# Performance work log

Measured on AMD Instinct MI355X. Metric: run time of the kernel, lower is better.

Reference implementation:

```python
import jax, jax.numpy as jnp
import numpy as np

DIM = 1024
DEPTH = 4
HEADS = 16
DHEAD = 64
INNER = HEADS * DHEAD  # 1024
FF = 4 * DIM           # 4096
SCALE = DHEAD ** -0.5
LS_INIT = 0.1          # LayerScale init_eps for depth <= 18


def _layernorm(x, w, b):
    mu = jnp.mean(x, axis=-1, keepdims=True)
    var = jnp.mean((x - mu) ** 2, axis=-1, keepdims=True)
    return (x - mu) / jnp.sqrt(var + 1e-5) * w + b


def setup_inputs() -> dict:
    key = jax.random.key(0)
    ks = jax.random.split(key, 6)
    s = 0.02
    return {
        "x": jax.random.normal(ks[0], (2, 1024, DIM), dtype=jnp.float32),
        "ln1_w": jnp.ones((DEPTH, DIM), jnp.float32),
        "ln1_b": jnp.zeros((DEPTH, DIM), jnp.float32),
        "w_qkv": jax.random.normal(ks[1], (DEPTH, DIM, 3 * INNER), jnp.float32) * s,
        "w_out": jax.random.normal(ks[2], (DEPTH, INNER, DIM), jnp.float32) * s,
        "b_out": jnp.zeros((DEPTH, DIM), jnp.float32),
        "ls1": jnp.full((DEPTH, DIM), LS_INIT, jnp.float32),
        "ln2_w": jnp.ones((DEPTH, DIM), jnp.float32),
        "ln2_b": jnp.zeros((DEPTH, DIM), jnp.float32),
        "w_ff1": jax.random.normal(ks[3], (DEPTH, DIM, 2 * FF), jnp.float32) * s,
        "b_ff1": jnp.zeros((DEPTH, 2 * FF), jnp.float32),
        "w_ff2": jax.random.normal(ks[4], (DEPTH, FF, DIM), jnp.float32) * s,
        "b_ff2": jnp.zeros((DEPTH, DIM), jnp.float32),
        "ls2": jnp.full((DEPTH, DIM), LS_INIT, jnp.float32),
    }


def _block(x, p):
    (ln1w, ln1b, wqkv, wout, bout, ls1,
     ln2w, ln2b, wff1, bff1, wff2, bff2, ls2) = p
    b, n, _ = x.shape
    # --- PreNorm + Attention (non-causal, no mask) + LayerScale, residual ---
    h = _layernorm(x, ln1w, ln1b)
    qkv = h @ wqkv                                   # [b, n, 3*inner]
    q, k, v = jnp.split(qkv, 3, axis=-1)
    def heads(t):
        return t.reshape(b, n, HEADS, DHEAD).transpose(0, 2, 1, 3)  # b h n d
    q, k, v = heads(q) * SCALE, heads(k), heads(v)
    dots = jnp.einsum("bhid,bhjd->bhij", q, k)       # full O(n^2) scores
    attn = jax.nn.softmax(dots, axis=-1)
    o = jnp.einsum("bhij,bhjd->bhid", attn, v)
    o = o.transpose(0, 2, 1, 3).reshape(b, n, INNER)
    o = o @ wout + bout
    x = x + o * ls1
    # --- PreNorm + GEGLU FeedForward + LayerScale, residual ---
    h = _layernorm(x, ln2w, ln2b)
    u = h @ wff1 + bff1                              # [b, n, 2*FF]
    a, g = jnp.split(u, 2, axis=-1)
    ff = (a * jax.nn.gelu(g, approximate=False)) @ wff2 + bff2
    x = x + ff * ls2
    return x, None


def reference(x, ln1_w, ln1_b, w_qkv, w_out, b_out, ls1,
              ln2_w, ln2_b, w_ff1, b_ff1, w_ff2, b_ff2, ls2):
    ps = (ln1_w, ln1_b, w_qkv, w_out, b_out, ls1,
          ln2_w, ln2_b, w_ff1, b_ff1, w_ff2, b_ff2, ls2)
    out, _ = jax.lax.scan(_block, x, ps)
    return out
```

## Files before the change

### kernel.cpp

```cpp
#include <hip/hip_runtime.h>
#include <cstdint>
#include <cstddef>

typedef __bf16 bf16_t;
typedef __bf16 bf16x8 __attribute__((ext_vector_type(8)));
typedef __bf16 bf16x4 __attribute__((ext_vector_type(4)));
typedef float  f32x4  __attribute__((ext_vector_type(4)));

#define DEV __device__ __forceinline__

static constexpr int   BATCH = 2;
static constexpr int   NTOK  = 1024;
static constexpr int   DIM   = 1024;
static constexpr int   MROWS = BATCH * NTOK;
static constexpr float SCALE = 0.125f;

DEV void load_lds16(const bf16_t* g, bf16_t* s) {
  __builtin_amdgcn_global_load_lds(
      (const __attribute__((address_space(1))) void*)g,
      (__attribute__((address_space(3))) void*)s, 16, 0, 0);
}

DEV float wave_sum(float v) {
#pragma unroll
  for (int m = 1; m < 64; m <<= 1) v += __shfl_xor(v, m, 64);
  return v;
}
DEV float block_sum(float v, float* sb) {
  v = wave_sum(v);
  __syncthreads();
  if ((threadIdx.x & 63) == 0) sb[threadIdx.x >> 6] = v;
  __syncthreads();
  return sb[0] + sb[1] + sb[2] + sb[3];
}

template <int BM, int BN, int WR, int WC, int MODE>
__global__ __launch_bounds__(256) void gemm_bt(
    const bf16_t* __restrict__ A, long sA0, long sA1, int lda,
    const bf16_t* __restrict__ B, long sB0, long sB1, int ldb,
    void* __restrict__ Cv, long sC0, long sC1, int ldc,
    int K, float alpha, const float* __restrict__ bias,
    const float* __restrict__ ls, bf16_t* __restrict__ vtp) {
  constexpr int TM = BM / WR / 16;
  constexpr int TN = BN / WC / 16;
  __shared__ __attribute__((aligned(16))) bf16_t As[BM * 32];
  __shared__ __attribute__((aligned(16))) bf16_t Bs[BN * 32];

  const int tid  = threadIdx.x;
  const int lane = tid & 63, wave = tid >> 6;
  const int z  = blockIdx.z;
  const int zh = z >> 4, zl = z & 15;
  A += (size_t)zh * sA0 + (size_t)zl * sA1;
  B += (size_t)zh * sB0 + (size_t)zl * sB1;

  const int m0 = blockIdx.y * BM, n0 = blockIdx.x * BN;
  const int wm = (wave / WC) * (BM / WR);
  const int wn = (wave % WC) * (BN / WC);
  const int fm = lane & 15, quad = lane >> 4;

  f32x4 acc[TM][TN] = {};

  for (int k0 = 0; k0 < K; k0 += 32) {
#pragma unroll
    for (int c = tid; c < BM * 4; c += 256) {
      const int row = c >> 2, kc = (c & 3) << 3;
      load_lds16(A + (size_t)(m0 + row) * lda + k0 + kc, &As[c * 8]);
    }
#pragma unroll
    for (int c = tid; c < BN * 4; c += 256) {
      const int row = c >> 2, kc = (c & 3) << 3;
      load_lds16(B + (size_t)(n0 + row) * ldb + k0 + kc, &Bs[c * 8]);
    }
    __syncthreads();

    bf16x8 af[TM], bfr[TN];
#pragma unroll
    for (int i = 0; i < TM; ++i)
      af[i] = *(const bf16x8*)&As[(wm + i * 16 + fm) * 32 + quad * 8];
#pragma unroll
    for (int j = 0; j < TN; ++j)
      bfr[j] = *(const bf16x8*)&Bs[(wn + j * 16 + fm) * 32 + quad * 8];
#pragma unroll
    for (int i = 0; i < TM; ++i)
#pragma unroll
      for (int j = 0; j < TN; ++j)
        acc[i][j] = __builtin_amdgcn_mfma_f32_16x16x32_bf16(af[i], bfr[j],
                                                            acc[i][j], 0, 0, 0);
    __syncthreads();
  }

  const size_t coff = (size_t)zh * sC0 + (size_t)zl * sC1;
  if constexpr (MODE == 3) {
    bf16_t* C = (bf16_t*)Cv;
#pragma unroll
    for (int i = 0; i < TM; ++i) {
      const int rowb = m0 + wm + i * 16 + quad * 4;
#pragma unroll
      for (int p = 0; p < TN / 2; ++p) {
        const int   cf = ((n0 + wn) >> 1) + p * 16 + fm;
        const float ba = bias[cf], bg = bias[4096 + cf];
#pragma unroll
        for (int r = 0; r < 4; ++r) {
          const float a  = acc[i][2 * p][r] + ba;
          const float g  = acc[i][2 * p + 1][r] + bg;
          const float ge = 0.5f * g * (1.f + erff(g * 0.70710678118654752f));
          C[(size_t)(rowb + r) * ldc + cf] = (bf16_t)(a * ge);
        }
      }
    }
  } else if constexpr (MODE == 4) {
    bf16_t* C = (bf16_t*)Cv;
#pragma unroll
    for (int i = 0; i < TM; ++i) {
#pragma unroll
      for (int j = 0; j < TN; ++j) {
        const int col  = n0 + wn + j * 16 + fm;
        const int rowb = m0 + wm + i * 16 + quad * 4;
        if (col < 2048) {
#pragma unroll
          for (int r = 0; r < 4; ++r)
            C[(size_t)(rowb + r) * ldc + col] = (bf16_t)acc[i][j][r];
        } else {
          const int hh = (col - 2048) >> 6, d = (col - 2048) & 63;
#pragma unroll
          for (int r = 0; r < 4; ++r) {
            const int row = rowb + r, bb = row >> 10, tok = row & 1023;
            vtp[((size_t)(bb * 16 + hh) * 64 + d) * 1024 + tok] =
                (bf16_t)acc[i][j][r];
          }
        }
      }
    }
  } else {
#pragma unroll
    for (int i = 0; i < TM; ++i) {
#pragma unroll
      for (int j = 0; j < TN; ++j) {
        const int col  = n0 + wn + j * 16 + fm;
        const int rowb = m0 + wm + i * 16 + quad * 4;
#pragma unroll
        for (int r = 0; r < 4; ++r) {
          const float  v   = acc[i][j][r];
          const size_t idx = coff + (size_t)(rowb + r) * ldc + col;
          if constexpr (MODE == 0) {
            ((bf16_t*)Cv)[idx] = (bf16_t)(v * alpha);
          } else if constexpr (MODE == 1) {
            ((bf16_t*)Cv)[idx] = (bf16_t)(v + bias[col]);
          } else {
            float* C = (float*)Cv;
            C[idx]   = C[idx] + (v + bias[col]) * ls[col];
          }
        }
      }
    }
  }
}

__global__ __launch_bounds__(256) void flash_attn(
    const bf16_t* __restrict__ qkv,
    const bf16_t* __restrict__ vT,
    bf16_t* __restrict__ o) {
  constexpr int NT = 128;
  __shared__ __attribute__((aligned(16))) bf16_t Qs[2 * 64 * 32];
  __shared__ __attribute__((aligned(16))) bf16_t Ks[2 * NT * 32];
  __shared__ __attribute__((aligned(16))) bf16_t Vs[4 * 64 * 32];
  __shared__ __attribute__((aligned(16))) bf16_t Ps[4][4 * 16 * 32];

  const int tid = threadIdx.x, lane = tid & 63, wave = tid >> 6;
  const int fm = lane & 15, quad = lane >> 4;
  const int z = blockIdx.y, b = z >> 4, h = z & 15;
  const int q0 = blockIdx.x * 64;
  const bf16_t* qb  = qkv + (size_t)b * 1024 * 3072 + h * 64;
  const bf16_t* kb  = qb + 1024;
  const bf16_t* vtb = vT + (size_t)z * 64 * 1024;

  for (int c = tid; c < 512; c += 256) {
    const int kk = c >> 8, rr = (c >> 2) & 63, ii = c & 3;
    load_lds16(qb + (size_t)(q0 + rr) * 3072 + kk * 32 + ii * 8, &Qs[c * 8]);
  }
  __syncthreads();
  bf16x8 qf[2];
  qf[0] = *(const bf16x8*)&Qs[(wave * 16 + fm) * 32 + quad * 8];
  qf[1] = *(const bf16x8*)&Qs[64 * 32 + (wave * 16 + fm) * 32 + quad * 8];

  float mr[4], lr[4];
  f32x4 oacc[4];
#pragma unroll
  for (int r = 0; r < 4; ++r) { mr[r] = -1e30f; lr[r] = 0.f; }
#pragma unroll
  for (int t = 0; t < 4; ++t) oacc[t] = (f32x4){0.f, 0.f, 0.f, 0.f};

  for (int kv0 = 0; kv0 < 1024; kv0 += NT) {
    __syncthreads();
    for (int c = tid; c < NT * 8; c += 256) {
      const int kk = c >> 9, rr = (c >> 2) & 127, ii = c & 3;
      load_lds16(kb + (size_t)(kv0 + rr) * 3072 + kk * 32 + ii * 8, &Ks[c * 8]);
    }
    for (int c = tid; c < 1024; c += 256) {
      const int tc = c >> 8, rr = (c >> 2) & 63, ii = c & 3;
      load_lds16(vtb + (size_t)rr * 1024 + kv0 + tc * 32 + ii * 8, &Vs[c * 8]);
    }
    __syncthreads();

    f32x4 sc[8];
#pragma unroll
    for (int nt = 0; nt < 8; ++nt) {
      sc[nt] = (f32x4){0.f, 0.f, 0.f, 0.f};
#pragma unroll
      for (int kk = 0; kk < 2; ++kk) {
        const bf16x8 kf =
            *(const bf16x8*)&Ks[kk * NT * 32 + (nt * 16 + fm) * 32 + quad * 8];
        sc[nt] = __builtin_amdgcn_mfma_f32_16x16x32_bf16(qf[kk], kf, sc[nt],
                                                         0, 0, 0);
      }
    }
    float tmax[4] = {-1e30f, -1e30f, -1e30f, -1e30f};
#pragma unroll
    for (int nt = 0; nt < 8; ++nt)
#pragma unroll
      for (int r = 0; r < 4; ++r) {
        sc[nt][r] *= SCALE;
        tmax[r] = fmaxf(tmax[r], sc[nt][r]);
      }
#pragma unroll
    for (int m = 1; m < 16; m <<= 1)
#pragma unroll
      for (int r = 0; r < 4; ++r)
        tmax[r] = fmaxf(tmax[r], __shfl_xor(tmax[r], m, 64));
    float alpha[4], mn[4], ps[4];
#pragma unroll
    for (int r = 0; r < 4; ++r) {
      mn[r]    = fmaxf(mr[r], tmax[r]);
      alpha[r] = __expf(mr[r] - mn[r]);
      mr[r]    = mn[r];
      ps[r]    = 0.f;
    }
#pragma unroll
    for (int nt = 0; nt < 8; ++nt) {
      const int tcol = nt * 16 + fm, kk = tcol >> 5, tw = tcol & 31;
#pragma unroll
      for (int r = 0; r < 4; ++r) {
        const float p = __expf(sc[nt][r] - mn[r]);
        ps[r] += p;
        Ps[wave][kk * 512 + (quad * 4 + r) * 32 + tw] = (bf16_t)p;
      }
    }
#pragma unroll
    for (int m = 1; m < 16; m <<= 1)
#pragma unroll
      for (int r = 0; r < 4; ++r) ps[r] += __shfl_xor(ps[r], m, 64);
#pragma unroll
    for (int r = 0; r < 4; ++r) lr[r] = lr[r] * alpha[r] + ps[r];
#pragma unroll
    for (int t = 0; t < 4; ++t)
#pragma unroll
      for (int r = 0; r < 4; ++r) oacc[t][r] *= alpha[r];
    __builtin_amdgcn_s_waitcnt(0xC07F);
#pragma unroll
    for (int kk = 0; kk < 4; ++kk) {
      const bf16x8 af =
          *(const bf16x8*)&Ps[wave][kk * 512 + fm * 32 + quad * 8];
#pragma unroll
      for (int t = 0; t < 4; ++t) {
        const bf16x8 vf =
            *(const bf16x8*)&Vs[kk * 64 * 32 + (t * 16 + fm) * 32 + quad * 8];
        oacc[t] = __builtin_amdgcn_mfma_f32_16x16x32_bf16(af, vf, oacc[t],
                                                          0, 0, 0);
      }
    }
  }

  const size_t orow0 = (size_t)b * 1024 + q0 + wave * 16 + quad * 4;
#pragma unroll
  for (int t = 0; t < 4; ++t) {
    const int col = h * 64 + t * 16 + fm;
#pragma unroll
    for (int r = 0; r < 4; ++r)
      o[(orow0 + r) * 1024 + col] = (bf16_t)(oacc[t][r] / lr[r]);
  }
}

__global__ __launch_bounds__(256) void transpose_all(
    const float* __restrict__ wqkv, const float* __restrict__ wout,
    const float* __restrict__ wff1, const float* __restrict__ wff2,
    bf16_t* __restrict__ wqkvT, bf16_t* __restrict__ woutT,
    bf16_t* __restrict__ wff1T, bf16_t* __restrict__ wff2T, int l) {
  __shared__ float t[32][33];
  int bx = blockIdx.x;
  const float* W;
  bf16_t*      WT;
  int N, K;
  bool perm = false;
  if (bx < 3072) {
    W = wqkv + (size_t)l * 1024 * 3072; WT = wqkvT; K = 1024; N = 3072;
  } else if (bx < 4096) {
    bx -= 3072;
    W = wout + (size_t)l * 1024 * 1024; WT = woutT; K = 1024; N = 1024;
  } else if (bx < 12288) {
    bx -= 4096;
    W = wff1 + (size_t)l * 1024 * 8192; WT = wff1T; K = 1024; N = 8192;
    perm = true;
  } else {
    bx -= 12288;
    W = wff2 + (size_t)l * 4096 * 1024; WT = wff2T; K = 4096; N = 1024;
  }
  const int nbx = N >> 5;
  const int n0 = (bx % nbx) * 32, k0 = (bx / nbx) * 32;
  const int tx = threadIdx.x & 31, ty = threadIdx.x >> 5;
#pragma unroll
  for (int s = 0; s < 4; ++s)
    t[ty + 8 * s][tx] = W[(size_t)(k0 + ty + 8 * s) * N + n0 + tx];
  __syncthreads();
#pragma unroll
  for (int s = 0; s < 4; ++s) {
    const int n = n0 + ty + 8 * s;
    int r;
    if (perm)
      r = (n < 4096) ? (((n >> 4) << 5) + (n & 15))
                     : ((((n - 4096) >> 4) << 5) + 16 + (n & 15));
    else
      r = n;
    WT[(size_t)r * K + k0 + tx] = (bf16_t)t[tx][ty + 8 * s];
  }
}

__global__ __launch_bounds__(256) void ln_kernel(const float* __restrict__ x,
                                                 const float* __restrict__ w,
                                                 const float* __restrict__ b,
                                                 bf16_t* __restrict__ out) {
  __shared__ float sb[4];
  const int row = blockIdx.x, tid = threadIdx.x;
  const float4 v = ((const float4*)(x + (size_t)row * DIM))[tid];
  float s = v.x + v.y + v.z + v.w;
  s = block_sum(s, sb);
  const float mu = s * (1.f / DIM);
  const float dx = v.x - mu, dy = v.y - mu, dz = v.z - mu, dw = v.w - mu;
  float q = dx * dx + dy * dy + dz * dz + dw * dw;
  q = block_sum(q, sb);
  const float rstd = rsqrtf(q * (1.f / DIM) + 1e-5f);
  const float4 wv = ((const float4*)w)[tid];
  const float4 bv = ((const float4*)b)[tid];
  bf16x4 o;
  o[0] = (bf16_t)(dx * rstd * wv.x + bv.x);
  o[1] = (bf16_t)(dy * rstd * wv.y + bv.y);
  o[2] = (bf16_t)(dz * rstd * wv.z + bv.z);
  o[3] = (bf16_t)(dw * rstd * wv.w + bv.w);
  ((bf16x4*)(out + (size_t)row * DIM))[tid] = o;
}

extern "C" void kernel_launch(void* const* d_in, const int* in_sizes, int n_in,
                              void* d_out, int out_size, void* d_ws,
                              size_t ws_size, hipStream_t stream) {
  const float* x_in = (const float*)d_in[0];
  const float* ln1w = (const float*)d_in[1];
  const float* ln1b = (const float*)d_in[2];
  const float* wqkv = (const float*)d_in[3];
  const float* wout = (const float*)d_in[4];
  const float* bout = (const float*)d_in[5];
  const float* ls1  = (const float*)d_in[6];
  const float* ln2w = (const float*)d_in[7];
  const float* ln2b = (const float*)d_in[8];
  const float* wff1 = (const float*)d_in[9];
  const float* bff1 = (const float*)d_in[10];
  const float* wff2 = (const float*)d_in[11];
  const float* bff2 = (const float*)d_in[12];
  const float* ls2  = (const float*)d_in[13];
  float*       xout = (float*)d_out;

  char*   ws     = (char*)d_ws;
  bf16_t* wqkvT  = (bf16_t*)ws; ws += (size_t)3072 * 1024 * 2;
  bf16_t* woutT  = (bf16_t*)ws; ws += (size_t)1024 * 1024 * 2;
  bf16_t* wff1T  = (bf16_t*)ws; ws += (size_t)8192 * 1024 * 2;
  bf16_t* wff2T  = (bf16_t*)ws; ws += (size_t)1024 * 4096 * 2;
  bf16_t* h_bf   = (bf16_t*)ws; ws += (size_t)MROWS * 1024 * 2;
  bf16_t* qkv_bf = (bf16_t*)ws; ws += (size_t)MROWS * 3072 * 2;
  bf16_t* o_bf   = (bf16_t*)ws; ws += (size_t)MROWS * 1024 * 2;
  bf16_t* vT     = (bf16_t*)ws; ws += (size_t)32 * 64 * 1024 * 2;
  bf16_t* ff_bf  = (bf16_t*)ws; ws += (size_t)MROWS * 4096 * 2;
  if (ws_size < (size_t)(ws - (char*)d_ws)) return;

  hipMemcpyAsync(xout, x_in, (size_t)MROWS * DIM * 4,
                 hipMemcpyDeviceToDevice, stream);

  for (int l = 0; l < 4; ++l) {
    transpose_all<<<dim3(16384), 256, 0, stream>>>(
        wqkv, wout, wff1, wff2, wqkvT, woutT, wff1T, wff2T, l);

    ln_kernel<<<MROWS, 256, 0, stream>>>(xout, ln1w + l * 1024,
                                         ln1b + l * 1024, h_bf);
    gemm_bt<128, 128, 2, 2, 4><<<dim3(24, 16, 1), 256, 0, stream>>>(
        h_bf, 0, 0, 1024, wqkvT, 0, 0, 1024, qkv_bf, 0, 0, 3072, 1024, 1.f,
        nullptr, nullptr, vT);
    flash_attn<<<dim3(16, 32), 256, 0, stream>>>(qkv_bf, vT, o_bf);
    gemm_bt<64, 128, 1, 4, 2><<<dim3(8, 32, 1), 256, 0, stream>>>(
        o_bf, 0, 0, 1024, woutT, 0, 0, 1024, xout, 0, 0, 1024, 1024, 1.f,
        bout + l * 1024, ls1 + l * 1024, nullptr);

    ln_kernel<<<MROWS, 256, 0, stream>>>(xout, ln2w + l * 1024,
                                         ln2b + l * 1024, h_bf);
    gemm_bt<128, 128, 2, 2, 3><<<dim3(64, 16, 1), 256, 0, stream>>>(
        h_bf, 0, 0, 1024, wff1T, 0, 0, 1024, ff_bf, 0, 0, 4096, 1024, 1.f,
        bff1 + l * 8192, nullptr, nullptr);
    gemm_bt<64, 128, 1, 4, 2><<<dim3(8, 32, 1), 256, 0, stream>>>(
        ff_bf, 0, 0, 4096, wff2T, 0, 0, 4096, xout, 0, 0, 1024, 4096, 1.f,
        bff2 + l * 1024, ls2 + l * 1024, nullptr);
  }
}
```

Before: 1.179 ms.

## Add 256x256 ping-pong pipelined GEMM kernel for GEGLU FF1 projection

Measured after the change: 1.134 ms. 3.8% less time.

```diff
diff --git a/kernel.cpp b/kernel.cpp
--- a/kernel.cpp
+++ b/kernel.cpp
@@ -90,25 +90,7 @@
   }
 
   const size_t coff = (size_t)zh * sC0 + (size_t)zl * sC1;
-  if constexpr (MODE == 3) {
-    bf16_t* C = (bf16_t*)Cv;
-#pragma unroll
-    for (int i = 0; i < TM; ++i) {
-      const int rowb = m0 + wm + i * 16 + quad * 4;
-#pragma unroll
-      for (int p = 0; p < TN / 2; ++p) {
-        const int   cf = ((n0 + wn) >> 1) + p * 16 + fm;
-        const float ba = bias[cf], bg = bias[4096 + cf];
-#pragma unroll
-        for (int r = 0; r < 4; ++r) {
-          const float a  = acc[i][2 * p][r] + ba;
-          const float g  = acc[i][2 * p + 1][r] + bg;
-          const float ge = 0.5f * g * (1.f + erff(g * 0.70710678118654752f));
-          C[(size_t)(rowb + r) * ldc + cf] = (bf16_t)(a * ge);
-        }
-      }
-    }
-  } else if constexpr (MODE == 4) {
+  if constexpr (MODE == 4) {
     bf16_t* C = (bf16_t*)Cv;
 #pragma unroll
     for (int i = 0; i < TM; ++i) {
@@ -151,6 +133,140 @@
             C[idx]   = C[idx] + (v + bias[col]) * ls[col];
           }
         }
+      }
+    }
+  }
+}
+
+__global__ __launch_bounds__(512, 2) void gemm256_ff1(
+    const bf16_t* __restrict__ A,
+    const bf16_t* __restrict__ B,
+    bf16_t* __restrict__ C,
+    const float* __restrict__ bias,
+    int K) {
+  __shared__ __attribute__((aligned(16))) bf16_t As[2][2][256 * 32];
+  __shared__ __attribute__((aligned(16))) bf16_t Bs[2][2][256 * 32];
+
+  const int tid = threadIdx.x, lane = tid & 63, wave = tid >> 6;
+  const int wm2 = wave >> 2, wn4 = wave & 3;
+  const int fm = lane & 15, quad = lane >> 4;
+  const int m0 = blockIdx.y * 256, n0 = blockIdx.x * 256;
+  const int NK = K >> 6;
+
+  auto stage = [&](const bf16_t* g, int base, int kt, int kh, bf16_t* s) {
+#pragma unroll
+    for (int it = 0; it < 2; ++it) {
+      const int c = it * 512 + tid, row = c >> 2, kc = (c & 3) << 3;
+      load_lds16(g + (size_t)(base + row) * K + kt * 64 + kh * 32 + kc,
+                 s + c * 8);
+    }
+  };
+
+  f32x4 acc[8][4] = {};
+
+  stage(A, m0, 0, 0, &As[0][0][0]);
+  stage(B, n0, 0, 0, &Bs[0][0][0]);
+  stage(A, m0, 0, 1, &As[0][1][0]);
+  stage(B, n0, 0, 1, &Bs[0][1][0]);
+  if (NK > 1) {
+    stage(A, m0, 1, 0, &As[1][0][0]);
+    stage(B, n0, 1, 0, &Bs[1][0][0]);
+    stage(A, m0, 1, 1, &As[1][1][0]);
+  }
+  asm volatile("s_waitcnt vmcnt(6)" ::: "memory");
+  __builtin_amdgcn_sched_barrier(0);
+  __builtin_amdgcn_s_barrier();
+
+  const int ar = wm2 * 128 + fm;
+  const int br = wn4 * 64 + fm;
+  const int qo = quad * 8;
+
+  for (int kt = 0; kt < NK; ++kt) {
+    const int cur = kt & 1;
+    bf16x8 af[8], b0, b1;
+
+#pragma unroll
+    for (int m = 0; m < 8; ++m)
+      af[m] = *(const bf16x8*)&As[cur][0][(ar + m * 16) * 32 + qo];
+    b0 = *(const bf16x8*)&Bs[cur][0][br * 32 + qo];
+    b1 = *(const bf16x8*)&Bs[cur][0][(br + 16) * 32 + qo];
+    if (kt + 1 < NK) stage(B, n0, kt + 1, 1, &Bs[cur ^ 1][1][0]);
+    __builtin_amdgcn_s_barrier();
+    __builtin_amdgcn_s_setprio(1);
+#pragma unroll
+    for (int m = 0; m < 8; ++m) {
+      acc[m][0] = __builtin_amdgcn_mfma_f32_16x16x32_bf16(af[m], b0,
+                                                          acc[m][0], 0, 0, 0);
+      acc[m][1] = __builtin_amdgcn_mfma_f32_16x16x32_bf16(af[m], b1,
+                                                          acc[m][1], 0, 0, 0);
+    }
+    __builtin_amdgcn_s_setprio(0);
+    __builtin_amdgcn_s_barrier();
+
+    b0 = *(const bf16x8*)&Bs[cur][0][(br + 32) * 32 + qo];
+    b1 = *(const bf16x8*)&Bs[cur][0][(br + 48) * 32 + qo];
+    if (kt + 2 < NK) stage(A, m0, kt + 2, 0, &As[cur][0][0]);
+    __builtin_amdgcn_s_barrier();
+    __builtin_amdgcn_s_setprio(1);
+#pragma unroll
+    for (int m = 0; m < 8; ++m) {
+      acc[m][2] = __builtin_amdgcn_mfma_f32_16x16x32_bf16(af[m], b0,
+                                                          acc[m][2], 0, 0, 0);
+      acc[m][3] = __builtin_amdgcn_mfma_f32_16x16x32_bf16(af[m], b1,
+                                                          acc[m][3], 0, 0, 0);
+    }
+    __builtin_amdgcn_s_setprio(0);
+    __builtin_amdgcn_s_barrier();
+
+#pragma unroll
+    for (int m = 0; m < 8; ++m)
+      af[m] = *(const bf16x8*)&As[cur][1][(ar + m * 16) * 32 + qo];
+    b0 = *(const bf16x8*)&Bs[cur][1][(br + 32) * 32 + qo];
+    b1 = *(const bf16x8*)&Bs[cur][1][(br + 48) * 32 + qo];
+    if (kt + 2 < NK) stage(B, n0, kt + 2, 0, &Bs[cur][0][0]);
+    __builtin_amdgcn_s_barrier();
+    __builtin_amdgcn_s_setprio(1);
+#pragma unroll
+    for (int m = 0; m < 8; ++m) {
+      acc[m][2] = __builtin_amdgcn_mfma_f32_16x16x32_bf16(af[m], b0,
+                                                          acc[m][2], 0, 0, 0);
+      acc[m][3] = __builtin_amdgcn_mfma_f32_16x16x32_bf16(af[m], b1,
+                                                          acc[m][3], 0, 0, 0);
+    }
+    __builtin_amdgcn_s_setprio(0);
+    __builtin_amdgcn_s_barrier();
+
+    b0 = *(const bf16x8*)&Bs[cur][1][br * 32 + qo];
+    b1 = *(const bf16x8*)&Bs[cur][1][(br + 16) * 32 + qo];
+    if (kt + 2 < NK) stage(A, m0, kt + 2, 1, &As[cur][1][0]);
+    asm volatile("s_waitcnt vmcnt(6)" ::: "memory");
+    __builtin_amdgcn_sched_barrier(0);
+    __builtin_amdgcn_s_barrier();
+    __builtin_amdgcn_s_setprio(1);
+#pragma unroll
+    for (int m = 0; m < 8; ++m) {
+      acc[m][0] = __builtin_amdgcn_mfma_f32_16x16x32_bf16(af[m], b0,
+                                                          acc[m][0], 0, 0, 0);
+      acc[m][1] = __builtin_amdgcn_mfma_f32_16x16x32_bf16(af[m], b1,
+                                                          acc[m][1], 0, 0, 0);
+    }
+    __builtin_amdgcn_s_setprio(0);
+    __builtin_amdgcn_s_barrier();
+  }
+
+#pragma unroll
+  for (int m = 0; m < 8; ++m) {
+    const int rowb = m0 + wm2 * 128 + m * 16 + quad * 4;
+#pragma unroll
+    for (int p = 0; p < 2; ++p) {
+      const int   cf = ((n0 + wn4 * 64 + p * 32) >> 1) + fm;
+      const float ba = bias[cf], bg = bias[4096 + cf];
+#pragma unroll
+      for (int r = 0; r < 4; ++r) {
+        const float a  = acc[m][2 * p][r] + ba;
+        const float g  = acc[m][2 * p + 1][r] + bg;
+        const float ge = 0.5f * g * (1.f + erff(g * 0.70710678118654752f));
+        C[(size_t)(rowb + r) * 4096 + cf] = (bf16_t)(a * ge);
       }
     }
   }
@@ -398,9 +514,8 @@
 
     ln_kernel<<<MROWS, 256, 0, stream>>>(xout, ln2w + l * 1024,
                                          ln2b + l * 1024, h_bf);
-    gemm_bt<128, 128, 2, 2, 3><<<dim3(64, 16, 1), 256, 0, stream>>>(
-        h_bf, 0, 0, 1024, wff1T, 0, 0, 1024, ff_bf, 0, 0, 4096, 1024, 1.f,
-        bff1 + l * 8192, nullptr, nullptr);
+    gemm256_ff1<<<dim3(32, 8), 512, 0, stream>>>(
+        h_bf, wff1T, ff_bf, bff1 + l * 8192, 1024);
     gemm_bt<64, 128, 1, 4, 2><<<dim3(8, 32, 1), 256, 0, stream>>>(
         ff_bf, 0, 0, 4096, wff2T, 0, 0, 4096, xout, 0, 0, 1024, 4096, 1.f,
         bff2 + l * 1024, ls2 + l * 1024, nullptr);
```
